# Performance work log

Measured on AMD Instinct MI355X. Metric: run time of the kernel, lower is better.

## Reference

```python
import jax, jax.numpy as jnp
import numpy as np

NUM_HEADS = 16


def rotate_half(x):
    half = x.shape[-1] // 2
    return jnp.concatenate((-x[..., half:], x[..., :half]), axis=-1)


def rope_tables(seq_len, head_dim, dtype=jnp.float32):
    inv_freq = 1.0 / (10000.0 ** (jnp.arange(0, head_dim, 2, dtype=jnp.float32) / head_dim))
    t = jnp.arange(seq_len, dtype=jnp.float32)
    freqs = jnp.outer(t, inv_freq)                 # [S, hd/2]
    emb = jnp.concatenate((freqs, freqs), axis=-1)  # [S, hd]
    return jnp.cos(emb).astype(dtype), jnp.sin(emb).astype(dtype)


def setup_inputs() -> dict:
    key = jax.random.key(0)
    k1, k2, k3 = jax.random.split(key, 3)
    B, S, D = 2, 2048, 1024
    x = jax.random.normal(k1, (B, S, D), dtype=jnp.float32)
    # causal lower-triangular mask, broadcast over batch/heads
    mask = jnp.tril(jnp.ones((S, S), dtype=bool))[None, None, :, :]
    w_qkv = jax.random.normal(k2, (3 * D, D), dtype=jnp.float32) * (D ** -0.5)
    w_out = jax.random.normal(k3, (D, D), dtype=jnp.float32) * (D ** -0.5)
    return {"x": x, "mask": mask, "w_qkv": w_qkv, "w_out": w_out}


def reference(x, mask, w_qkv, w_out):
    B, S, D = x.shape
    H = NUM_HEADS
    hd = D // H
    scale = hd ** -0.5

    qkv = jnp.einsum('bsd,ed->bse', x, w_qkv)          # [B, S, 3D]
    q, k, v = jnp.split(qkv, 3, axis=-1)

    def split(t):
        return t.reshape(B, S, H, hd).transpose(0, 2, 1, 3)  # [B, H, S, hd]

    q, k, v = split(q), split(k), split(v)

    cos, sin = rope_tables(S, hd, x.dtype)             # [S, hd]
    cos = cos[None, None]
    sin = sin[None, None]
    q = q * cos + rotate_half(q) * sin
    k = k * cos + rotate_half(k) * sin

    attn = jnp.einsum('bhqd,bhkd->bhqk', q, k) * scale  # [B, H, S, S]
    attn = jnp.where(mask, attn, jnp.float32(-jnp.inf).astype(attn.dtype))
    attn = jax.nn.softmax(attn, axis=-1)
    out = jnp.einsum('bhqk,bhkd->bhqd', attn, v)        # [B, H, S, hd]
    out = out.transpose(0, 2, 1, 3).reshape(B, S, D)
    return jnp.einsum('bsd,ed->bse', out, w_out)
```

## Files before the change

### kernel.cpp

```cpp
#include <hip/hip_runtime.h>
#include <hip/hip_bf16.h>

typedef __attribute__((ext_vector_type(8))) __bf16 bf16x8;
typedef __attribute__((ext_vector_type(4))) __bf16 bf16x4;
typedef __attribute__((ext_vector_type(2))) __bf16 bf16x2;
typedef __attribute__((ext_vector_type(4))) float f32x4;
typedef __attribute__((ext_vector_type(16))) float f32x16;

#define SEQ 2048
#define NH 16
#define HD 64
#define DMODEL 1024
#define BATCH 2
#define MTOT 4096
#define NCH 36

__device__ __forceinline__ void gl_lds16(const void* g, void* l) {
    __builtin_amdgcn_global_load_lds(
        (const __attribute__((address_space(1))) void*)(uintptr_t)g,
        (__attribute__((address_space(3))) void*)(uintptr_t)l,
        16, 0, 0);
}

__device__ __forceinline__ unsigned pk2(float x, float y) {
    union { bf16x2 h; unsigned u; } c;
    c.h = bf16x2{ (__bf16)x, (__bf16)y };
    return c.u;
}

__global__ __launch_bounds__(256) void cast3(const float4* __restrict__ x,
                                             const float4* __restrict__ wq,
                                             const float4* __restrict__ wo,
                                             __bf16* __restrict__ xb,
                                             __bf16* __restrict__ wqb,
                                             __bf16* __restrict__ wob) {
    const int NX  = 1024 * 1024;
    const int NWQ = 768 * 1024;
    const int NTOT = NX + NWQ + 256 * 1024;
    int i = blockIdx.x * 256 + threadIdx.x;
    if (i >= NTOT) return;
    float4 v; __bf16* dst; int j;
    if (i < NX)            { j = i;            v = x[j];  dst = xb;  }
    else if (i < NX + NWQ) { j = i - NX;       v = wq[j]; dst = wqb; }
    else                   { j = i - NX - NWQ; v = wo[j]; dst = wob; }
    bf16x4 o = { (__bf16)v.x, (__bf16)v.y, (__bf16)v.z, (__bf16)v.w };
    *(bf16x4*)(dst + (size_t)j * 4) = o;
}

__global__ __launch_bounds__(256) void gemm_qkv(const __bf16* __restrict__ A,
                                                const __bf16* __restrict__ Bt,
                                                __bf16* __restrict__ Qp,
                                                __bf16* __restrict__ Kp,
                                                __bf16* __restrict__ Vt) {
    const int K = 1024;
    __shared__ __bf16 sA[128 * 64];
    __shared__ __bf16 sB[128 * 64];
    const int tid = threadIdx.x, lane = tid & 63, wave = tid >> 6;
    const int lrow = lane & 15, quad = lane >> 4;
    const int m0 = blockIdx.y * 128, n0 = blockIdx.x * 128;
    const int wm = wave >> 1, wn = wave & 1;

    const __bf16* ap[4]; const __bf16* bp[4]; int ldso[4];
#pragma unroll
    for (int i = 0; i < 4; ++i) {
        int r0 = i * 32 + wave * 8;
        int row = r0 + (lane >> 3);
        int cg = (lane & 7) ^ (row & 7);
        ap[i] = A + (size_t)(m0 + row) * K + cg * 8;
        bp[i] = Bt + (size_t)(n0 + row) * K + cg * 8;
        ldso[i] = r0 * 128;
    }
    int arow[4], brow[4];
#pragma unroll
    for (int i = 0; i < 4; ++i) {
        arow[i] = wm * 64 + i * 16 + lrow;
        brow[i] = wn * 64 + i * 16 + lrow;
    }

    f32x4 z = {0.f, 0.f, 0.f, 0.f};
    f32x4 acc[4][4];
#pragma unroll
    for (int i = 0; i < 4; ++i)
#pragma unroll
        for (int j = 0; j < 4; ++j) acc[i][j] = z;

    char* sAb = (char*)sA; char* sBb = (char*)sB;
    for (int k0 = 0; k0 < K; k0 += 64) {
#pragma unroll
        for (int i = 0; i < 4; ++i) gl_lds16(ap[i] + k0, sAb + ldso[i]);
#pragma unroll
        for (int i = 0; i < 4; ++i) gl_lds16(bp[i] + k0, sBb + ldso[i]);
        __syncthreads();
#pragma unroll
        for (int ks = 0; ks < 2; ++ks) {
            bf16x8 af[4], bfr[4];
#pragma unroll
            for (int i = 0; i < 4; ++i)
                af[i] = *(const bf16x8*)(sAb + arow[i] * 128 +
                                         (((ks * 4 + quad) ^ (arow[i] & 7)) << 4));
#pragma unroll
            for (int i = 0; i < 4; ++i)
                bfr[i] = *(const bf16x8*)(sBb + brow[i] * 128 +
                                          (((ks * 4 + quad) ^ (brow[i] & 7)) << 4));
#pragma unroll
            for (int i = 0; i < 4; ++i)
#pragma unroll
                for (int j = 0; j < 4; ++j)
                    acc[i][j] = __builtin_amdgcn_mfma_f32_16x16x32_bf16(
                        af[i], bfr[j], acc[i][j], 0, 0, 0);
        }
        __syncthreads();
    }

    const int nt = blockIdx.x;
    const int sec = nt >> 3;
    const int b = m0 >> 11;
    const int s0b = m0 & (SEQ - 1);
    const int h = (nt & 7) * 2 + wn;
    const int bh = b * NH + h;

    if (sec < 2) {
        const float scale = sec ? 1.0f : 0.18033688011112042f;
        __bf16* dst = sec ? Kp : Qp;
        float invf0 = 0.15915494309189535f *
                      exp2f(-(float)lrow * 0.4152410118609203f);
        float invf1 = invf0 * 0.01f;
#pragma unroll
        for (int i = 0; i < 4; ++i) {
            int srow0 = s0b + wm * 64 + i * 16 + quad * 4;
#pragma unroll
            for (int j = 0; j < 2; ++j) {
                float invf = j ? invf1 : invf0;
#pragma unroll
                for (int r = 0; r < 4; ++r) {
                    int s = srow0 + r;
                    float rev = (float)s * invf;
                    float fr = rev - floorf(rev);
                    float sn = __builtin_amdgcn_sinf(fr);
                    float cs = __builtin_amdgcn_cosf(fr);
                    float lo = acc[i][j][r], hi = acc[i][j + 2][r];
                    float olo = (lo * cs - hi * sn) * scale;
                    float ohi = (hi * cs + lo * sn) * scale;
                    size_t base = ((size_t)bh * SEQ + s) * HD + j * 16 + lrow;
                    dst[base] = (__bf16)olo;
                    dst[base + 32] = (__bf16)ohi;
                }
            }
        }
    } else {
#pragma unroll
        for (int i = 0; i < 4; ++i) {
            int srow0 = s0b + wm * 64 + i * 16 + quad * 4;
#pragma unroll
            for (int j = 0; j < 4; ++j) {
                int ch = j * 16 + lrow;
                bf16x4 wv = { (__bf16)acc[i][j][0], (__bf16)acc[i][j][1],
                              (__bf16)acc[i][j][2], (__bf16)acc[i][j][3] };
                *(bf16x4*)(Vt + ((size_t)bh * HD + ch) * SEQ + srow0) = wv;
            }
        }
    }
}

__global__ __launch_bounds__(256) void gemm_bt(const __bf16* __restrict__ A,
                                               const __bf16* __restrict__ Bt,
                                               float* __restrict__ Cf,
                                               int M, int N, int K) {
    __shared__ __bf16 sA[128 * 64];
    __shared__ __bf16 sB[128 * 64];
    const int tid = threadIdx.x, lane = tid & 63, wave = tid >> 6;
    const int lrow = lane & 15, quad = lane >> 4;
    const int m0 = blockIdx.y * 128, n0 = blockIdx.x * 128;
    const int wm = wave >> 1, wn = wave & 1;
    const int nz = gridDim.z;
    const int Kh = K / nz;
    const int kbeg = blockIdx.z * Kh, kend = kbeg + Kh;

    const __bf16* ap[4]; const __bf16* bp[4]; int ldso[4];
#pragma unroll
    for (int i = 0; i < 4; ++i) {
        int r0 = i * 32 + wave * 8;
        int row = r0 + (lane >> 3);
        int cg = (lane & 7) ^ (row & 7);
        ap[i] = A + (size_t)(m0 + row) * K + cg * 8;
        bp[i] = Bt + (size_t)(n0 + row) * K + cg * 8;
        ldso[i] = r0 * 128;
    }
    int arow[4], brow[4];
#pragma unroll
    for (int i = 0; i < 4; ++i) {
        arow[i] = wm * 64 + i * 16 + lrow;
        brow[i] = wn * 64 + i * 16 + lrow;
    }

    f32x4 z = {0.f, 0.f, 0.f, 0.f};
    f32x4 acc[4][4];
#pragma unroll
    for (int i = 0; i < 4; ++i)
#pragma unroll
        for (int j = 0; j < 4; ++j) acc[i][j] = z;

    char* sAb = (char*)sA; char* sBb = (char*)sB;
    for (int k0 = kbeg; k0 < kend; k0 += 64) {
#pragma unroll
        for (int i = 0; i < 4; ++i) gl_lds16(ap[i] + k0, sAb + ldso[i]);
#pragma unroll
        for (int i = 0; i < 4; ++i) gl_lds16(bp[i] + k0, sBb + ldso[i]);
        __syncthreads();
#pragma unroll
        for (int ks = 0; ks < 2; ++ks) {
            bf16x8 af[4], bfr[4];
#pragma unroll
            for (int i = 0; i < 4; ++i)
                af[i] = *(const bf16x8*)(sAb + arow[i] * 128 +
                                         (((ks * 4 + quad) ^ (arow[i] & 7)) << 4));
#pragma unroll
            for (int i = 0; i < 4; ++i)
                bfr[i] = *(const bf16x8*)(sBb + brow[i] * 128 +
                                          (((ks * 4 + quad) ^ (brow[i] & 7)) << 4));
#pragma unroll
            for (int i = 0; i < 4; ++i)
#pragma unroll
                for (int j = 0; j < 4; ++j)
                    acc[i][j] = __builtin_amdgcn_mfma_f32_16x16x32_bf16(
                        af[i], bfr[j], acc[i][j], 0, 0, 0);
        }
        __syncthreads();
    }
#pragma unroll
    for (int i = 0; i < 4; ++i)
#pragma unroll
        for (int j = 0; j < 4; ++j)
#pragma unroll
            for (int r = 0; r < 4; ++r) {
                int row = m0 + wm * 64 + i * 16 + quad * 4 + r;
                int col = n0 + wn * 64 + j * 16 + lrow;
                if (nz > 1) atomicAdd(&Cf[(size_t)row * N + col], acc[i][j][r]);
                else        Cf[(size_t)row * N + col] = acc[i][j][r];
            }
}

__global__ __launch_bounds__(256) void flash_attn(const __bf16* __restrict__ Qp,
                                                  const __bf16* __restrict__ Kp,
                                                  const __bf16* __restrict__ Vtp,
                                                  __bf16* __restrict__ Aout,
                                                  __bf16* __restrict__ Opart,
                                                  float* __restrict__ Lpart) {
    __shared__ __bf16 sK[128 * 64];
    __shared__ __bf16 sV[2][64 * 64];

    const int tid = threadIdx.x, lane = tid & 63, wave = tid >> 6;
    const int ql = lane & 31, half = lane >> 5;
    const int bh = blockIdx.x;
    const int c = blockIdx.y;
    int qt, C, ci;
    if (c < 4)       { qt = c;                 C = 1; ci = 0; }
    else if (c < 12) { qt = 4 + ((c - 4) >> 1); C = 2; ci = (c - 4) & 1; }
    else if (c < 24) { int d = c - 12; qt = 8 + d / 3; C = 3; ci = d % 3; }
    else             { int d = c - 24; qt = 12 + (d >> 2); C = 4; ci = d & 3; }
    const int kt0 = ((qt + 1) * ci) / C;
    const int kt1 = ((qt + 1) * (ci + 1)) / C;

    const int b = bh >> 4, hh = bh & 15;
    const int q0 = qt * 128;
    const int qrow = q0 + wave * 32 + ql;

    bf16x8 qf[4];
    const __bf16* qb = Qp + ((size_t)bh * SEQ + qrow) * HD + half * 8;
#pragma unroll
    for (int kc = 0; kc < 4; ++kc) qf[kc] = *(const bf16x8*)(qb + kc * 16);

    const __bf16* kp[4]; int kldso[4];
    const __bf16* vp[4]; int vldso[4];
#pragma unroll
    for (int i = 0; i < 4; ++i) {
        int r0 = i * 32 + wave * 8;
        int row = r0 + (lane >> 3);
        int cg = (lane & 7) ^ (row & 7);
        kp[i] = Kp + ((size_t)bh * SEQ + row) * HD + cg * 8;
        kldso[i] = r0 * 128;
        int s = i >> 1;
        int rv0 = (i & 1) * 32 + wave * 8;
        int vrow = rv0 + (lane >> 3);
        int vcg = (lane & 7) ^ (vrow & 7);
        vp[i] = Vtp + ((size_t)bh * HD + vrow) * SEQ + s * 64 + vcg * 8;
        vldso[i] = s * 8192 + rv0 * 128;
    }

    char* sKb = (char*)sK;
    char* sVb = (char*)sV;

    f32x16 zz = {0.f};
    f32x16 o0 = zz, o1 = zz;
    float l = 0.f;

    for (int kt = kt0; kt < kt1; ++kt) {
        const int k0 = kt * 128;
#pragma unroll
        for (int i = 0; i < 4; ++i) gl_lds16(kp[i] + (size_t)k0 * HD, sKb + kldso[i]);
#pragma unroll
        for (int i = 0; i < 4; ++i) gl_lds16(vp[i] + k0, sVb + vldso[i]);
        __syncthreads();

        const bool diag = (kt == qt);
#pragma unroll
        for (int ktl = 0; ktl < 4; ++ktl) {
            int keyl = ktl * 32 + ql;
            f32x16 st = zz;
#pragma unroll
            for (int kc = 0; kc < 4; ++kc) {
                bf16x8 kf = *(const bf16x8*)(
                    sKb + keyl * 128 + (((kc * 2 + half) ^ (keyl & 7)) << 4));
                st = __builtin_amdgcn_mfma_f32_32x32x16_bf16(kf, qf[kc], st, 0, 0, 0);
            }

#pragma unroll
            for (int g = 0; g < 4; ++g)
#pragma unroll
                for (int t = 0; t < 4; ++t) {
                    float e = exp2f(st[g * 4 + t]);
                    if (diag) {
                        int key = k0 + ktl * 32 + 8 * g + 4 * half + t;
                        if (key > qrow) e = 0.f;
                    }
                    st[g * 4 + t] = e;
                    l += e;
                }

#pragma unroll
            for (int lo = 0; lo < 2; ++lo) {
                int base = lo * 8;
                unsigned a0 = pk2(st[base + 0], st[base + 1]);
                unsigned a1 = pk2(st[base + 2], st[base + 3]);
                unsigned b0 = pk2(st[base + 4], st[base + 5]);
                unsigned b1 = pk2(st[base + 6], st[base + 7]);
                unsigned d0, d1, d2, d3;
#if __has_builtin(__builtin_amdgcn_permlane32_swap)
                {
                    auto r0 = __builtin_amdgcn_permlane32_swap(a0, b0, false, false);
                    auto r1 = __builtin_amdgcn_permlane32_swap(a1, b1, false, false);
                    d0 = r0[0]; d2 = r0[1];
                    d1 = r1[0]; d3 = r1[1];
                }
#else
                {
                    unsigned z0 = half ? a0 : b0;
                    unsigned z1 = half ? a1 : b1;
                    unsigned x0 = (unsigned)__shfl_xor((int)z0, 32, 64);
                    unsigned x1 = (unsigned)__shfl_xor((int)z1, 32, 64);
                    d0 = half ? x0 : a0;
                    d1 = half ? x1 : a1;
                    d2 = half ? b0 : x0;
                    d3 = half ? b1 : x1;
                }
#endif
                union { unsigned u[4]; bf16x8 v; } pf;
                pf.u[0] = d0; pf.u[1] = d1; pf.u[2] = d2; pf.u[3] = d3;

                int kb = ktl * 2 + lo;
                int sV_off = (kb >> 2) * 8192;
                int cc = (kb & 3) * 2 + half;
                bf16x8 vf0 = *(const bf16x8*)(
                    sVb + sV_off + ql * 128 + ((cc ^ (ql & 7)) << 4));
                bf16x8 vf1 = *(const bf16x8*)(
                    sVb + sV_off + (32 + ql) * 128 + ((cc ^ (ql & 7)) << 4));
                o0 = __builtin_amdgcn_mfma_f32_32x32x16_bf16(vf0, pf.v, o0, 0, 0, 0);
                o1 = __builtin_amdgcn_mfma_f32_32x32x16_bf16(vf1, pf.v, o1, 0, 0, 0);
            }
        }
        __syncthreads();
    }

    l += __shfl_xor(l, 32, 64);
    if (C == 1) {
        float invl = 1.0f / l;
        __bf16* obase = Aout + ((size_t)b * SEQ + qrow) * DMODEL + hh * HD;
#pragma unroll
        for (int g = 0; g < 4; ++g) {
            bf16x4 w0 = { (__bf16)(o0[g*4+0]*invl), (__bf16)(o0[g*4+1]*invl),
                          (__bf16)(o0[g*4+2]*invl), (__bf16)(o0[g*4+3]*invl) };
            bf16x4 w1 = { (__bf16)(o1[g*4+0]*invl), (__bf16)(o1[g*4+1]*invl),
                          (__bf16)(o1[g*4+2]*invl), (__bf16)(o1[g*4+3]*invl) };
            *(bf16x4*)(obase + 8 * g + 4 * half) = w0;
            *(bf16x4*)(obase + 32 + 8 * g + 4 * half) = w1;
        }
    } else {
        int cidx = c - 4;
        __bf16* ob = Opart + ((size_t)(bh * NCH + cidx) << 13) +
                     (wave * 32 + ql) * 64;
#pragma unroll
        for (int g = 0; g < 4; ++g) {
            bf16x4 w0 = { (__bf16)o0[g*4+0], (__bf16)o0[g*4+1],
                          (__bf16)o0[g*4+2], (__bf16)o0[g*4+3] };
            bf16x4 w1 = { (__bf16)o1[g*4+0], (__bf16)o1[g*4+1],
                          (__bf16)o1[g*4+2], (__bf16)o1[g*4+3] };
            *(bf16x4*)(ob + 8 * g + 4 * half) = w0;
            *(bf16x4*)(ob + 32 + 8 * g + 4 * half) = w1;
        }
        if (!half)
            Lpart[(bh * NCH + cidx) * 128 + wave * 32 + ql] = l;
    }
}

__global__ __launch_bounds__(256) void combine(const __bf16* __restrict__ Opart,
                                               const float* __restrict__ Lpart,
                                               __bf16* __restrict__ Aout) {
    const int bh = blockIdx.x, qt = 4 + blockIdx.y;
    const int C = (qt + 4) >> 2;
    const int cbase = (qt < 8) ? (qt - 4) * 2
                     : (qt < 12) ? 8 + (qt - 8) * 3
                                 : 20 + (qt - 12) * 4;
    const int t = threadIdx.x;
    const int row = t >> 1, hcol = (t & 1) * 32;
    float acc[32];
#pragma unroll
    for (int i = 0; i < 32; ++i) acc[i] = 0.f;
    float l = 0.f;
    for (int ci = 0; ci < C; ++ci) {
        int ch = bh * NCH + cbase + ci;
        l += Lpart[ch * 128 + row];
        const __bf16* p = Opart + ((size_t)ch << 13) + row * 64 + hcol;
#pragma unroll
        for (int k4 = 0; k4 < 4; ++k4) {
            bf16x8 v = ((const bf16x8*)p)[k4];
#pragma unroll
            for (int j = 0; j < 8; ++j) acc[k4 * 8 + j] += (float)v[j];
        }
    }
    float invl = 1.0f / l;
    const int b = bh >> 4, hh = bh & 15;
    __bf16* dst = Aout + ((size_t)(b * SEQ + qt * 128 + row)) * DMODEL +
                  hh * 64 + hcol;
#pragma unroll
    for (int k4 = 0; k4 < 4; ++k4) {
        bf16x8 w;
#pragma unroll
        for (int j = 0; j < 8; ++j) w[j] = (__bf16)(acc[k4 * 8 + j] * invl);
        ((bf16x8*)dst)[k4] = w;
    }
}

extern "C" void kernel_launch(void* const* d_in, const int* in_sizes, int n_in,
                              void* d_out, int out_size, void* d_ws, size_t ws_size,
                              hipStream_t stream) {
    (void)in_sizes; (void)n_in; (void)out_size; (void)ws_size;
    const float* x  = (const float*)d_in[0];
    const float* wq = (const float*)d_in[2];
    const float* wo = (const float*)d_in[3];
    float* out = (float*)d_out;

    char* w = (char*)d_ws;
    __bf16* xb   = (__bf16*)(w);
    __bf16* wqb  = (__bf16*)(w + (8ull << 20));
    __bf16* wob  = (__bf16*)(w + (14ull << 20));
    __bf16* Opart= (__bf16*)(w + (16ull << 20));
    float*  Lpart= (float*) (w + (35ull << 20));
    __bf16* Qb   = (__bf16*)(w + (40ull << 20));
    __bf16* Kb   = (__bf16*)(w + (48ull << 20));
    __bf16* Vtb  = (__bf16*)(w + (56ull << 20));
    __bf16* aob  = xb;

    cast3<<<8192, 256, 0, stream>>>((const float4*)x, (const float4*)wq,
                                    (const float4*)wo, xb, wqb, wob);
    gemm_qkv<<<dim3(24, 32), 256, 0, stream>>>(xb, wqb, Qb, Kb, Vtb);
    flash_attn<<<dim3(32, 40), 256, 0, stream>>>(Qb, Kb, Vtb, aob, Opart, Lpart);
    combine<<<dim3(32, 12), 256, 0, stream>>>(Opart, Lpart, aob);
    hipMemsetAsync(out, 0, (size_t)MTOT * DMODEL * 4, stream);
    gemm_bt<<<dim3(8, 32, 2), 256, 0, stream>>>(aob, wob, out,
                                                MTOT, 1024, 1024);
}
```

Before: 216.8 us.

## Rebalance attention chunking via table, drop split-K out-proj and permlane swap

Replaces the formula-based split of causal query tiles into key chunks with a constant lookup table that gives 32 chunks of roughly equal work per head, down from 40 uneven chunks, and shrinks the combine grid to match. The output projection GEMM no longer uses split-K with atomics, so the memset and the atomic adds go away. The P·V step now packs probabilities directly and loads V fragments as two 8-byte halves instead of exchanging across half-waves with permlane swaps, which changes the LDS access pattern. Fewer attention blocks and a non-split GEMM with 256 blocks may leave the GPU less fully occupied.

After: 201.6 us. -7.0%, faster.

```diff
diff --git a/kernel.cpp b/kernel.cpp
--- a/kernel.cpp
+++ b/kernel.cpp
@@ -13,7 +13,7 @@
 #define DMODEL 1024
 #define BATCH 2
 #define MTOT 4096
-#define NCH 36
+#define NCH 26
 
 __device__ __forceinline__ void gl_lds16(const void* g, void* l) {
     __builtin_amdgcn_global_load_lds(
@@ -27,6 +27,18 @@
     c.h = bf16x2{ (__bf16)x, (__bf16)y };
     return c.u;
 }
+
+__constant__ int4 FCHUNK[32] = {
+    {0,0,1,-1},{1,0,2,-1},{2,0,3,-1},{3,0,4,-1},{4,0,5,-1},{5,0,6,-1},
+    {6,0,4,0},{6,4,7,1},{7,0,4,2},{7,4,8,3},
+    {8,0,5,4},{8,5,9,5},{9,0,5,6},{9,5,10,7},
+    {10,0,6,8},{10,6,11,9},
+    {11,0,4,10},{11,4,8,11},{11,8,12,12},
+    {12,0,5,13},{12,5,9,14},{12,9,13,15},
+    {13,0,5,16},{13,5,10,17},{13,10,14,18},
+    {14,0,5,19},{14,5,10,20},{14,10,15,21},
+    {15,0,4,22},{15,4,8,23},{15,8,12,24},{15,12,16,25}
+};
 
 __global__ __launch_bounds__(256) void cast3(const float4* __restrict__ x,
                                              const float4* __restrict__ wq,
@@ -172,9 +184,6 @@
     const int lrow = lane & 15, quad = lane >> 4;
     const int m0 = blockIdx.y * 128, n0 = blockIdx.x * 128;
     const int wm = wave >> 1, wn = wave & 1;
-    const int nz = gridDim.z;
-    const int Kh = K / nz;
-    const int kbeg = blockIdx.z * Kh, kend = kbeg + Kh;
 
     const __bf16* ap[4]; const __bf16* bp[4]; int ldso[4];
 #pragma unroll
@@ -201,7 +210,7 @@
         for (int j = 0; j < 4; ++j) acc[i][j] = z;
 
     char* sAb = (char*)sA; char* sBb = (char*)sB;
-    for (int k0 = kbeg; k0 < kend; k0 += 64) {
+    for (int k0 = 0; k0 < K; k0 += 64) {
 #pragma unroll
         for (int i = 0; i < 4; ++i) gl_lds16(ap[i] + k0, sAb + ldso[i]);
 #pragma unroll
@@ -235,8 +244,7 @@
             for (int r = 0; r < 4; ++r) {
                 int row = m0 + wm * 64 + i * 16 + quad * 4 + r;
                 int col = n0 + wn * 64 + j * 16 + lrow;
-                if (nz > 1) atomicAdd(&Cf[(size_t)row * N + col], acc[i][j][r]);
-                else        Cf[(size_t)row * N + col] = acc[i][j][r];
+                Cf[(size_t)row * N + col] = acc[i][j][r];
             }
 }
 
@@ -252,14 +260,8 @@
     const int tid = threadIdx.x, lane = tid & 63, wave = tid >> 6;
     const int ql = lane & 31, half = lane >> 5;
     const int bh = blockIdx.x;
-    const int c = blockIdx.y;
-    int qt, C, ci;
-    if (c < 4)       { qt = c;                 C = 1; ci = 0; }
-    else if (c < 12) { qt = 4 + ((c - 4) >> 1); C = 2; ci = (c - 4) & 1; }
-    else if (c < 24) { int d = c - 12; qt = 8 + d / 3; C = 3; ci = d % 3; }
-    else             { int d = c - 24; qt = 12 + (d >> 2); C = 4; ci = d & 3; }
-    const int kt0 = ((qt + 1) * ci) / C;
-    const int kt1 = ((qt + 1) * (ci + 1)) / C;
+    const int4 chd = FCHUNK[blockIdx.y];
+    const int qt = chd.x, kt0 = chd.y, kt1 = chd.z, cs = chd.w;
 
     const int b = bh >> 4, hh = bh & 15;
     const int q0 = qt * 128;
@@ -315,64 +317,45 @@
             }
 
 #pragma unroll
-            for (int g = 0; g < 4; ++g)
-#pragma unroll
-                for (int t = 0; t < 4; ++t) {
-                    float e = exp2f(st[g * 4 + t]);
-                    if (diag) {
-                        int key = k0 + ktl * 32 + 8 * g + 4 * half + t;
-                        if (key > qrow) e = 0.f;
-                    }
-                    st[g * 4 + t] = e;
-                    l += e;
-                }
+            for (int i = 0; i < 16; ++i) st[i] = exp2f(st[i]);
+            if (diag) {
+                int kbase = k0 + ktl * 32 + 4 * half;
+#pragma unroll
+                for (int g = 0; g < 4; ++g)
+#pragma unroll
+                    for (int t = 0; t < 4; ++t)
+                        if (kbase + 8 * g + t > qrow) st[g * 4 + t] = 0.f;
+            }
+#pragma unroll
+            for (int i = 0; i < 16; ++i) l += st[i];
 
 #pragma unroll
             for (int lo = 0; lo < 2; ++lo) {
-                int base = lo * 8;
-                unsigned a0 = pk2(st[base + 0], st[base + 1]);
-                unsigned a1 = pk2(st[base + 2], st[base + 3]);
-                unsigned b0 = pk2(st[base + 4], st[base + 5]);
-                unsigned b1 = pk2(st[base + 6], st[base + 7]);
-                unsigned d0, d1, d2, d3;
-#if __has_builtin(__builtin_amdgcn_permlane32_swap)
-                {
-                    auto r0 = __builtin_amdgcn_permlane32_swap(a0, b0, false, false);
-                    auto r1 = __builtin_amdgcn_permlane32_swap(a1, b1, false, false);
-                    d0 = r0[0]; d2 = r0[1];
-                    d1 = r1[0]; d3 = r1[1];
-                }
-#else
-                {
-                    unsigned z0 = half ? a0 : b0;
-                    unsigned z1 = half ? a1 : b1;
-                    unsigned x0 = (unsigned)__shfl_xor((int)z0, 32, 64);
-                    unsigned x1 = (unsigned)__shfl_xor((int)z1, 32, 64);
-                    d0 = half ? x0 : a0;
-                    d1 = half ? x1 : a1;
-                    d2 = half ? b0 : x0;
-                    d3 = half ? b1 : x1;
-                }
-#endif
                 union { unsigned u[4]; bf16x8 v; } pf;
-                pf.u[0] = d0; pf.u[1] = d1; pf.u[2] = d2; pf.u[3] = d3;
+#pragma unroll
+                for (int d = 0; d < 4; ++d)
+                    pf.u[d] = pk2(st[lo * 8 + 2 * d], st[lo * 8 + 2 * d + 1]);
 
                 int kb = ktl * 2 + lo;
-                int sV_off = (kb >> 2) * 8192;
-                int cc = (kb & 3) * 2 + half;
-                bf16x8 vf0 = *(const bf16x8*)(
-                    sVb + sV_off + ql * 128 + ((cc ^ (ql & 7)) << 4));
-                bf16x8 vf1 = *(const bf16x8*)(
-                    sVb + sV_off + (32 + ql) * 128 + ((cc ^ (ql & 7)) << 4));
-                o0 = __builtin_amdgcn_mfma_f32_32x32x16_bf16(vf0, pf.v, o0, 0, 0, 0);
-                o1 = __builtin_amdgcn_mfma_f32_32x32x16_bf16(vf1, pf.v, o1, 0, 0, 0);
+                int sv = (kb >> 2) * 8192;
+                int c0 = (kb & 3) * 2, c1 = c0 + 1;
+                union { bf16x4 h[2]; bf16x8 v; } vf0, vf1;
+                int r0b = ql * 128, r1b = (32 + ql) * 128;
+                int x0 = ((c0 ^ (ql & 7)) << 4) + 8 * half;
+                int x1 = ((c1 ^ (ql & 7)) << 4) + 8 * half;
+                vf0.h[0] = *(const bf16x4*)(sVb + sv + r0b + x0);
+                vf0.h[1] = *(const bf16x4*)(sVb + sv + r0b + x1);
+                vf1.h[0] = *(const bf16x4*)(sVb + sv + r1b + x0);
+                vf1.h[1] = *(const bf16x4*)(sVb + sv + r1b + x1);
+                o0 = __builtin_amdgcn_mfma_f32_32x32x16_bf16(vf0.v, pf.v, o0, 0, 0, 0);
+                o1 = __builtin_amdgcn_mfma_f32_32x32x16_bf16(vf1.v, pf.v, o1, 0, 0, 0);
             }
         }
         __syncthreads();
     }
 
     l += __shfl_xor(l, 32, 64);
-    if (C == 1) {
+    if (cs < 0) {
         float invl = 1.0f / l;
         __bf16* obase = Aout + ((size_t)b * SEQ + qrow) * DMODEL + hh * HD;
 #pragma unroll
@@ -385,8 +368,7 @@
             *(bf16x4*)(obase + 32 + 8 * g + 4 * half) = w1;
         }
     } else {
-        int cidx = c - 4;
-        __bf16* ob = Opart + ((size_t)(bh * NCH + cidx) << 13) +
+        __bf16* ob = Opart + ((size_t)(bh * NCH + cs) << 13) +
                      (wave * 32 + ql) * 64;
 #pragma unroll
         for (int g = 0; g < 4; ++g) {
@@ -398,18 +380,18 @@
             *(bf16x4*)(ob + 32 + 8 * g + 4 * half) = w1;
         }
         if (!half)
-            Lpart[(bh * NCH + cidx) * 128 + wave * 32 + ql] = l;
+            Lpart[(bh * NCH + cs) * 128 + wave * 32 + ql] = l;
     }
 }
 
 __global__ __launch_bounds__(256) void combine(const __bf16* __restrict__ Opart,
                                                const float* __restrict__ Lpart,
                                                __bf16* __restrict__ Aout) {
-    const int bh = blockIdx.x, qt = 4 + blockIdx.y;
-    const int C = (qt + 4) >> 2;
-    const int cbase = (qt < 8) ? (qt - 4) * 2
-                     : (qt < 12) ? 8 + (qt - 8) * 3
-                                 : 20 + (qt - 12) * 4;
+    const int bh = blockIdx.x, qy = blockIdx.y;
+    const int qt = 6 + qy;
+    const int Ct[10] = {2,2,2,2,2,3,3,3,3,4};
+    const int cb[10] = {0,2,4,6,8,10,13,16,19,22};
+    const int C = Ct[qy], cbase = cb[qy];
     const int t = threadIdx.x;
     const int row = t >> 1, hcol = (t & 1) * 32;
     float acc[32];
@@ -463,9 +445,7 @@
     cast3<<<8192, 256, 0, stream>>>((const float4*)x, (const float4*)wq,
                                     (const float4*)wo, xb, wqb, wob);
     gemm_qkv<<<dim3(24, 32), 256, 0, stream>>>(xb, wqb, Qb, Kb, Vtb);
-    flash_attn<<<dim3(32, 40), 256, 0, stream>>>(Qb, Kb, Vtb, aob, Opart, Lpart);
-    combine<<<dim3(32, 12), 256, 0, stream>>>(Opart, Lpart, aob);
-    hipMemsetAsync(out, 0, (size_t)MTOT * DMODEL * 4, stream);
-    gemm_bt<<<dim3(8, 32, 2), 256, 0, stream>>>(aob, wob, out,
-                                                MTOT, 1024, 1024);
-}
+    flash_attn<<<dim3(32, 32), 256, 0, stream>>>(Qb, Kb, Vtb, aob, Opart, Lpart);
+    combine<<<dim3(32, 10), 256, 0, stream>>>(Opart, Lpart, aob);
+    gemm_bt<<<dim3(8, 32), 256, 0, stream>>>(aob, wob, out, MTOT, 1024, 1024);
+}
```
